# Kernel optimization log

Measured on AMD Instinct MI355X. Metric: run time of the kernel, lower is better.

Reference implementation:

```python
import jax, jax.numpy as jnp
import numpy as np

B, T, F = 16384, 48, 4
UNITS = 256
OUT_STEPS = 24


def setup_inputs() -> dict:
    key = jax.random.key(0)
    ks = jax.random.split(key, 6)
    s_x = 1.0 / np.sqrt(F)
    s_h = 1.0 / np.sqrt(UNITS)
    return {
        "x": jax.random.normal(ks[0], (B, T, F), jnp.float32),
        "Wx": jax.random.normal(ks[1], (F, 4 * UNITS), jnp.float32) * s_x,
        "Wh": jax.random.normal(ks[2], (UNITS, 4 * UNITS), jnp.float32) * s_h,
        "b": jnp.zeros((4 * UNITS,), jnp.float32),
        "Wd": jax.random.normal(ks[3], (UNITS, F), jnp.float32) * s_h,
        "bd": jnp.zeros((F,), jnp.float32),
    }


def _lstm_cell(xt, h, c, Wx, Wh, b):
    # Keras LSTMCell gate order: i, f, g(cell candidate), o
    z = xt @ Wx + h @ Wh + b  # [B, 4*units]
    i, f, g, o = jnp.split(z, 4, axis=-1)
    i = jax.nn.sigmoid(i)
    f = jax.nn.sigmoid(f)
    g = jnp.tanh(g)
    o = jax.nn.sigmoid(o)
    c_new = f * c + i * g
    h_new = o * jnp.tanh(c_new)
    return h_new, c_new


def reference(x, Wx, Wh, b, Wd, bd):
    bsz = x.shape[0]
    h0 = jnp.zeros((bsz, UNITS), x.dtype)
    c0 = jnp.zeros((bsz, UNITS), x.dtype)

    # --- warmup: run LSTM over the input window, keep final state ---
    def warm_step(carry, xt):
        h, c = carry
        h, c = _lstm_cell(xt, h, c, Wx, Wh, b)
        return (h, c), None

    (h, c), _ = jax.lax.scan(warm_step, (h0, c0), jnp.swapaxes(x, 0, 1))
    pred0 = h @ Wd + bd  # first prediction [B, F]

    def ar_step(carry, _):
        h, c, pred = carry
        h, c = _lstm_cell(pred, h, c, Wx, Wh, b)
        pred = h @ Wd + bd
        return (h, c, pred), pred

    _, preds = jax.lax.scan(ar_step, (h, c, pred0), None, length=OUT_STEPS - 1)
    preds = jnp.concatenate([pred0[None], preds], axis=0)  # [out_steps, B, F]
    return jnp.swapaxes(preds, 0, 1)  # [B, out_steps, F]
```

## Files before the change

### kernel.cpp

```cpp
#include <hip/hip_runtime.h>


typedef unsigned short u16;
typedef __attribute__((ext_vector_type(8))) short bf16x8;
typedef __attribute__((ext_vector_type(4))) float f32x4;
typedef __attribute__((ext_vector_type(16))) float f32x16;

#define PITCH 296
#define HB 18944
#define WARM 48
#define STEPS 71
#define LOG2E  1.442695041f
#define LOG2E2 2.885390082f

__device__ __forceinline__ u16 f2bf(float f) {
    unsigned u = __float_as_uint(f);
    u += 0x7FFFu + ((u >> 16) & 1u);
    return (u16)(u >> 16);
}

__device__ __forceinline__ unsigned pk_bf16(float a, float b) {
    unsigned d;
    asm("v_cvt_pk_bf16_f32 %0, %1, %2" : "=v"(d) : "v"(a), "v"(b));
    return d;
}

__device__ __forceinline__ void sync_lds() {
    asm volatile("s_waitcnt lgkmcnt(0)\n\ts_barrier" ::: "memory");
}

__global__ void prep_weights(const float* __restrict__ Wx,
                             const float* __restrict__ Wh,
                             const float* __restrict__ b,
                             const float* __restrict__ Wd,
                             const float* __restrict__ bd,
                             u16* __restrict__ whext,
                             u16* __restrict__ wdp) {
    int idx = blockIdx.x * 256 + threadIdx.x;
    if (idx < 34816) {
        int lane = idx & 63;
        int fr = idx >> 6;
        int g = fr & 3;
        int wv = (fr >> 2) & 7;
        int kt = fr >> 5;
        int k0 = kt * 16 + (lane >> 5) * 8;
        int n = 256 * g + 32 * wv + (lane & 31);
        float sc = (g == 2) ? LOG2E2 : LOG2E;
        u16 v[8];
#pragma unroll
        for (int j = 0; j < 8; ++j) {
            int k = k0 + j;
            float f = 0.0f;
            if (k < 256) f = Wh[k * 1024 + n];
            else if (k < 260) f = Wx[(k - 256) * 1024 + n];
            else if (k == 260) f = b[n];
            v[j] = f2bf(f * sc);
        }
        ushort4* dst = (ushort4*)(whext + (size_t)idx * 8);
        dst[0] = make_ushort4(v[0], v[1], v[2], v[3]);
        dst[1] = make_ushort4(v[4], v[5], v[6], v[7]);
    } else if (idx < 34816 + 576) {
        int id2 = idx - 34816;
        int lane = id2 & 63;
        int kc = id2 >> 6;
        int m = lane & 15;
        int k0 = kc * 32 + (lane >> 4) * 8;
        u16 v[8];
#pragma unroll
        for (int j = 0; j < 8; ++j) {
            int k = k0 + j;
            float f = 0.0f;
            if (m < 4) {
                if (k < 256) f = Wd[k * 4 + m];
                else if (k == 260) f = bd[m];
            }
            v[j] = f2bf(f);
        }
        ushort4* dst = (ushort4*)(wdp + (size_t)id2 * 8);
        dst[0] = make_ushort4(v[0], v[1], v[2], v[3]);
        dst[1] = make_ushort4(v[4], v[5], v[6], v[7]);
    }
}

#define WL(DST, T) do {                                                       \
    const char* _p = wpw + ((size_t)(T) << 15);                               \
    DST[0] = *(const bf16x8*)(_p + voffl);                                    \
    DST[1] = *(const bf16x8*)(_p + voffl + 1024);                             \
    DST[2] = *(const bf16x8*)(_p + voffl + 2048);                             \
    DST[3] = *(const bf16x8*)(_p + voffl + 3072);                             \
} while (0)

#define HL(DST, T) do {                                                       \
    DST[0] = *(const bf16x8*)&hr[hrow0 + (T) * 16];                           \
    DST[1] = *(const bf16x8*)&hr[hrow1 + (T) * 16];                           \
} while (0)

#define MT(WA, HBX)                                                           \
    _Pragma("unroll") for (int m = 0; m < 2; ++m)                             \
    _Pragma("unroll") for (int g = 0; g < 4; ++g)                             \
        acc[m][g] = __builtin_amdgcn_mfma_f32_32x32x16_bf16(                  \
            WA[g], HBX[m], acc[m][g], 0, 0, 0);

#define STG(K, AW, HBX) do { MT(AW, HBX); WL(AW, (K) + 3); HL(HBX, (K) + 2); } while (0)

__global__ __launch_bounds__(512, 2) void lstm_main(
    const float* __restrict__ x, const u16* __restrict__ whext,
    const u16* __restrict__ wdp, float* __restrict__ out) {
    __shared__ __align__(16) u16 hbuf[2 * HB];

    const int tid = threadIdx.x;
    const int w = tid >> 6;
    const int l = tid & 63;
    const int l31 = l & 31;
    const int lh = l >> 5;
    const long long rowBase = (long long)blockIdx.x * 64;

    {
        int4 z = make_int4(0, 0, 0, 0);
        for (int i = tid; i < 4736; i += 512) ((int4*)hbuf)[i] = z;
    }
    sync_lds();
    if (tid < 64) {
        hbuf[tid * PITCH + 260] = (u16)0x3F80;
        hbuf[HB + tid * PITCH + 260] = (u16)0x3F80;
        const float4 xv = *(const float4*)(x + (rowBase + tid) * 192);
        uint2* p = (uint2*)&hbuf[tid * PITCH + 256];
        *p = make_uint2(pk_bf16(xv.x, xv.y), pk_bf16(xv.z, xv.w));
    }

    const char* __restrict__ wpw = (const char*)whext + (size_t)w * 4096;
    const char* __restrict__ dp = (const char*)wdp;
    const int voffl = l * 16;
    const int hrow0 = l31 * PITCH + lh * 8;
    const int hrow1 = (32 + l31) * PITCH + lh * 8;

    f32x16 c[2] = {};
    bf16x8 aw0[4], aw1[4], aw2[4];
    WL(aw0, 0);
    WL(aw1, 1);
    WL(aw2, 2);

    for (int step = 0; step < STEPS; ++step) {
        const u16* hr = hbuf + (step & 1) * HB;
        u16* hw = hbuf + ((step & 1) ^ 1) * HB;

        float4 xv = make_float4(0.f, 0.f, 0.f, 0.f);
        if (w == 0 && step < WARM - 1)
            xv = *(const float4*)(x + (rowBase + l) * 192 + (step + 1) * 4);

        sync_lds();

        f32x16 acc[2][4] = {};
        bf16x8 hb0[2], hb1[2];
        HL(hb0, 0);
        HL(hb1, 1);

        STG(0, aw0, hb0);
        STG(1, aw1, hb1);
#pragma unroll 1
        for (int k = 2; k < 14; k += 6) {
            STG(k + 0, aw2, hb0);
            STG(k + 1, aw0, hb1);
            STG(k + 2, aw1, hb0);
            STG(k + 3, aw2, hb1);
            STG(k + 4, aw0, hb0);
            STG(k + 5, aw1, hb1);
        }
        MT(aw2, hb0); WL(aw2, 2); HL(hb0, 16);
        MT(aw0, hb1); WL(aw0, 0);
        MT(aw1, hb0); WL(aw1, 1);

#pragma unroll
        for (int m = 0; m < 2; ++m) {
            const int hwrow = (32 * m + l31) * PITCH + 32 * w + 4 * lh;
#pragma unroll
            for (int q = 0; q < 4; ++q) {
                unsigned pk[2];
#pragma unroll
                for (int hp = 0; hp < 2; ++hp) {
                    float h2[2];
#pragma unroll
                    for (int rr = 0; rr < 2; ++rr) {
                        const int r = q * 4 + hp * 2 + rr;
                        float ei = __builtin_amdgcn_exp2f(-acc[m][0][r]);
                        float ef = __builtin_amdgcn_exp2f(-acc[m][1][r]);
                        float eg = __builtin_amdgcn_exp2f(-acc[m][2][r]);
                        float eo = __builtin_amdgcn_exp2f(-acc[m][3][r]);
                        float ai = 1.0f + ei, af = 1.0f + ef;
                        float ag = 1.0f + eg, ao = 1.0f + eo;
                        float P  = ai * ag;
                        float rD = __builtin_amdgcn_rcpf(P * af);
                        float cn = fmaf(c[m][r] * P, rD, (1.0f - eg) * af * rD);
                        c[m][r] = cn;
                        float ec = __builtin_amdgcn_exp2f(-LOG2E2 * cn);
                        float rE = __builtin_amdgcn_rcpf(ao * (1.0f + ec));
                        h2[rr] = (1.0f - ec) * rE;
                    }
                    pk[hp] = pk_bf16(h2[0], h2[1]);
                }
                *(uint2*)&hw[hwrow + 8 * q] = make_uint2(pk[0], pk[1]);
            }
        }

        if (step < WARM - 1) {
            if (w == 0) {
                uint2* p = (uint2*)&hw[l * PITCH + 256];
                *p = make_uint2(pk_bf16(xv.x, xv.y), pk_bf16(xv.z, xv.w));
            }
        } else {
            sync_lds();
            if (w < 4) {
                f32x4 pacc = {};
                const int col = l & 15;
                const int prow = (16 * w + col) * PITCH + (l >> 4) * 8;
#pragma unroll
                for (int kc = 0; kc < 9; ++kc) {
                    bf16x8 hbp = *(const bf16x8*)&hw[prow + kc * 32];
                    bf16x8 wap = *(const bf16x8*)(dp + ((size_t)kc * 64 + l) * 16);
                    pacc = __builtin_amdgcn_mfma_f32_16x16x32_bf16(wap, hbp, pacc, 0, 0, 0);
                }
                if ((l >> 4) == 0) {
                    int s = step - (WARM - 1);
                    int batch = 16 * w + col;
                    *(float4*)&out[((rowBase + batch) * 24 + s) * 4] =
                        make_float4(pacc[0], pacc[1], pacc[2], pacc[3]);
                    *(uint2*)&hw[batch * PITCH + 256] =
                        make_uint2(pk_bf16(pacc[0], pacc[1]), pk_bf16(pacc[2], pacc[3]));
                }
            }
        }
    }
}

extern "C" void kernel_launch(void* const* d_in, const int* in_sizes, int n_in,
                              void* d_out, int out_size, void* d_ws, size_t ws_size,
                              hipStream_t stream) {
    const float* x  = (const float*)d_in[0];
    const float* Wx = (const float*)d_in[1];
    const float* Wh = (const float*)d_in[2];
    const float* b  = (const float*)d_in[3];
    const float* Wd = (const float*)d_in[4];
    const float* bd = (const float*)d_in[5];
    float* out = (float*)d_out;

    u16* whext = (u16*)d_ws;
    u16* wdp = (u16*)((char*)d_ws + 557056);

    prep_weights<<<(34816 + 576 + 255) / 256, 256, 0, stream>>>(Wx, Wh, b, Wd, bd, whext, wdp);
    lstm_main<<<256, 512, 0, stream>>>(x, whext, wdp, out);
}
```

Measured before the change: 744.3 us.

## Move dense projection into next step and replace barrier with LDS flag wait

The output projection for autoregressive steps now runs at the start of the next step on the same buffer the step reads, instead of after a second block-wide barrier at the end of each step. The four projecting waves publish per-wave counters in LDS. The other waves spin on those counters only just before loading the last K tile, which holds the input columns, so the remaining MFMA tiles can overlap the projection. A final projection after the loop writes the last output step. This removes one block barrier per AR step, at the cost of relying on volatile LDS spin-waits for ordering.

```diff
diff --git a/kernel.cpp b/kernel.cpp
--- a/kernel.cpp
+++ b/kernel.cpp
@@ -27,6 +27,17 @@
 
 __device__ __forceinline__ void sync_lds() {
     asm volatile("s_waitcnt lgkmcnt(0)\n\ts_barrier" ::: "memory");
+}
+
+__device__ __forceinline__ void wait4(const int* f, int tgt) {
+    for (;;) {
+        int a = ((volatile const int*)f)[0];
+        int b = ((volatile const int*)f)[1];
+        int c = ((volatile const int*)f)[2];
+        int d = ((volatile const int*)f)[3];
+        if (a >= tgt && b >= tgt && c >= tgt && d >= tgt) break;
+    }
+    asm volatile("" ::: "memory");
 }
 
 __global__ void prep_weights(const float* __restrict__ Wx,
@@ -107,6 +118,7 @@
     const float* __restrict__ x, const u16* __restrict__ whext,
     const u16* __restrict__ wdp, float* __restrict__ out) {
     __shared__ __align__(16) u16 hbuf[2 * HB];
+    __shared__ int flag16[4];
 
     const int tid = threadIdx.x;
     const int w = tid >> 6;
@@ -118,6 +130,7 @@
     {
         int4 z = make_int4(0, 0, 0, 0);
         for (int i = tid; i < 4736; i += 512) ((int4*)hbuf)[i] = z;
+        if (tid < 4) flag16[tid] = 0;
     }
     sync_lds();
     if (tid < 64) {
@@ -142,6 +155,7 @@
 
     for (int step = 0; step < STEPS; ++step) {
         const u16* hr = hbuf + (step & 1) * HB;
+        u16* hrw = hbuf + (step & 1) * HB;
         u16* hw = hbuf + ((step & 1) ^ 1) * HB;
 
         float4 xv = make_float4(0.f, 0.f, 0.f, 0.f);
@@ -149,6 +163,28 @@
             xv = *(const float4*)(x + (rowBase + l) * 192 + (step + 1) * 4);
 
         sync_lds();
+
+        if (step >= WARM && w < 4) {
+            f32x4 pacc = {};
+            const int col = l & 15;
+            const int prow = (16 * w + col) * PITCH + (l >> 4) * 8;
+#pragma unroll
+            for (int kc = 0; kc < 9; ++kc) {
+                bf16x8 hbp = *(const bf16x8*)&hr[prow + kc * 32];
+                bf16x8 wap = *(const bf16x8*)(dp + ((size_t)kc * 64 + l) * 16);
+                pacc = __builtin_amdgcn_mfma_f32_16x16x32_bf16(wap, hbp, pacc, 0, 0, 0);
+            }
+            if ((l >> 4) == 0) {
+                int s = step - WARM;
+                int batch = 16 * w + col;
+                *(float4*)&out[((rowBase + batch) * 24 + s) * 4] =
+                    make_float4(pacc[0], pacc[1], pacc[2], pacc[3]);
+                *(uint2*)&hrw[batch * PITCH + 256] =
+                    make_uint2(pk_bf16(pacc[0], pacc[1]), pk_bf16(pacc[2], pacc[3]));
+            }
+            asm volatile("s_waitcnt lgkmcnt(0)" ::: "memory");
+            if (l == 0) *(volatile int*)&flag16[w] = step - WARM + 1;
+        }
 
         f32x16 acc[2][4] = {};
         bf16x8 hb0[2], hb1[2];
@@ -166,7 +202,9 @@
             STG(k + 4, aw0, hb0);
             STG(k + 5, aw1, hb1);
         }
-        MT(aw2, hb0); WL(aw2, 2); HL(hb0, 16);
+        MT(aw2, hb0); WL(aw2, 2);
+        if (step >= WARM) wait4(flag16, step - WARM + 1);
+        HL(hb0, 16);
         MT(aw0, hb1); WL(aw0, 0);
         MT(aw1, hb0); WL(aw1, 1);
 
@@ -207,27 +245,25 @@
                 uint2* p = (uint2*)&hw[l * PITCH + 256];
                 *p = make_uint2(pk_bf16(xv.x, xv.y), pk_bf16(xv.z, xv.w));
             }
-        } else {
-            sync_lds();
-            if (w < 4) {
-                f32x4 pacc = {};
-                const int col = l & 15;
-                const int prow = (16 * w + col) * PITCH + (l >> 4) * 8;
-#pragma unroll
-                for (int kc = 0; kc < 9; ++kc) {
-                    bf16x8 hbp = *(const bf16x8*)&hw[prow + kc * 32];
-                    bf16x8 wap = *(const bf16x8*)(dp + ((size_t)kc * 64 + l) * 16);
-                    pacc = __builtin_amdgcn_mfma_f32_16x16x32_bf16(wap, hbp, pacc, 0, 0, 0);
-                }
-                if ((l >> 4) == 0) {
-                    int s = step - (WARM - 1);
-                    int batch = 16 * w + col;
-                    *(float4*)&out[((rowBase + batch) * 24 + s) * 4] =
-                        make_float4(pacc[0], pacc[1], pacc[2], pacc[3]);
-                    *(uint2*)&hw[batch * PITCH + 256] =
-                        make_uint2(pk_bf16(pacc[0], pacc[1]), pk_bf16(pacc[2], pacc[3]));
-                }
-            }
+        }
+    }
+
+    sync_lds();
+    if (w < 4) {
+        const u16* hf = hbuf + (((STEPS - 1) & 1) ^ 1) * HB;
+        f32x4 pacc = {};
+        const int col = l & 15;
+        const int prow = (16 * w + col) * PITCH + (l >> 4) * 8;
+#pragma unroll
+        for (int kc = 0; kc < 9; ++kc) {
+            bf16x8 hbp = *(const bf16x8*)&hf[prow + kc * 32];
+            bf16x8 wap = *(const bf16x8*)(dp + ((size_t)kc * 64 + l) * 16);
+            pacc = __builtin_amdgcn_mfma_f32_16x16x32_bf16(wap, hbp, pacc, 0, 0, 0);
+        }
+        if ((l >> 4) == 0) {
+            int batch = 16 * w + col;
+            *(float4*)&out[((rowBase + batch) * 24 + 23) * 4] =
+                make_float4(pacc[0], pacc[1], pacc[2], pacc[3]);
         }
     }
 }
```

After: 742.8 us. About the same (-0.2%).
